# Performance work log

Measured on AMD Instinct MI355X. Metric: run time of the kernel, lower is better.

## Reference

```python
import jax, jax.numpy as jnp
import numpy as np

B, T, D, H, NH = 128, 64, 64, 128, 4


def setup_inputs() -> dict:
    key = jax.random.key(0)
    ks = jax.random.split(key, 32)
    s = 0.05
    inp = {
        "x": jax.random.normal(ks[0], (B, T, D), dtype=jnp.float32),
        "mask": jnp.ones((B, T), dtype=jnp.int32),
        # per-feature GRU params (input size 1, PyTorch gate order r,z,n)
        "Wih": jax.random.normal(ks[1], (D, 3 * H), dtype=jnp.float32) * s,
        "Whh": jax.random.normal(ks[2], (D, 3 * H, H), dtype=jnp.float32) * s,
        "bih": jax.random.normal(ks[3], (D, 3 * H), dtype=jnp.float32) * s,
        "bhh": jax.random.normal(ks[4], (D, 3 * H), dtype=jnp.float32) * s,
        # MHA projections (stored [in,out]; y = x @ W + b)
        "Wq": jax.random.normal(ks[5], (H, H), dtype=jnp.float32) * s,
        "bq": jnp.zeros((H,), dtype=jnp.float32),
        "Wk": jax.random.normal(ks[6], (H, H), dtype=jnp.float32) * s,
        "bk": jnp.zeros((H,), dtype=jnp.float32),
        "Wv": jax.random.normal(ks[7], (H, H), dtype=jnp.float32) * s,
        "bv": jnp.zeros((H,), dtype=jnp.float32),
        "Wo": jax.random.normal(ks[8], (H, H), dtype=jnp.float32) * s,
        "bo": jnp.zeros((H,), dtype=jnp.float32),
        # FFN
        "W1": jax.random.normal(ks[9], (H, 2 * H), dtype=jnp.float32) * s,
        "b1": jnp.zeros((2 * H,), dtype=jnp.float32),
        "W2": jax.random.normal(ks[10], (2 * H, H), dtype=jnp.float32) * s,
        "b2": jnp.zeros((H,), dtype=jnp.float32),
        # LayerNorms
        "g1": jnp.ones((H,), dtype=jnp.float32),
        "be1": jnp.zeros((H,), dtype=jnp.float32),
        "g2": jnp.ones((H,), dtype=jnp.float32),
        "be2": jnp.zeros((H,), dtype=jnp.float32),
        # FinalAttentionQKV
        "Fq": jax.random.normal(ks[11], (H, H), dtype=jnp.float32) * s,
        "fbq": jnp.zeros((H,), dtype=jnp.float32),
        "Fk": jax.random.normal(ks[12], (H, H), dtype=jnp.float32) * s,
        "fbk": jnp.zeros((H,), dtype=jnp.float32),
        "Fv": jax.random.normal(ks[13], (H, H), dtype=jnp.float32) * s,
        "fbv": jnp.zeros((H,), dtype=jnp.float32),
        "Fout": jax.random.normal(ks[14], (H,), dtype=jnp.float32) * s,
        "fbout": jnp.zeros((), dtype=jnp.float32),
    }
    return inp


def _layernorm(x, g, b, eps=1e-5):
    m = jnp.mean(x, axis=-1, keepdims=True)
    v = jnp.mean((x - m) ** 2, axis=-1, keepdims=True)
    return (x - m) * jax.lax.rsqrt(v + eps) * g + b


def _forward(x, mask, Wih, Whh, bih, bhh, Wq, bq, Wk, bk, Wv, bv, Wo, bo,
             W1, b1, W2, b2, g1, be1, g2, be2,
             Fq, fbq, Fk, fbk, Fv, fbv, Fout, fbout):
    Bc, Tc, Dc = x.shape
    Hc = Whh.shape[-1]

    # --- D independent GRUs, fused: batch axes (B, D), scalar input per step ---
    def step(h, xt):  # h: [B,D,H], xt: [B,D]
        gx = xt[..., None] * Wih + bih                     # [B,D,3H]
        gh = jnp.einsum('bdh,dkh->bdk', h, Whh) + bhh      # [B,D,3H]
        r = jax.nn.sigmoid(gx[..., :Hc] + gh[..., :Hc])
        z = jax.nn.sigmoid(gx[..., Hc:2 * Hc] + gh[..., Hc:2 * Hc])
        n = jnp.tanh(gx[..., 2 * Hc:] + r * gh[..., 2 * Hc:])
        hn = (1.0 - z) * n + z * h
        return hn, hn

    xs = jnp.transpose(x, (1, 0, 2))                        # [T,B,D]
    h0 = jnp.zeros((Bc, Dc, Hc), dtype=x.dtype)
    _, ys = jax.lax.scan(step, h0, xs)                      # [T,B,D,H]

    # last_by_lengths: gather hidden state at index lengths-1 per batch element
    lengths = jnp.sum(mask, axis=1)                         # [B]
    idx = jnp.clip(lengths - 1, 0, Tc - 1)
    emb = ys[idx, jnp.arange(Bc)]                           # [B,D,H] (D tokens)

    # --- MHA (self-attention over D feature tokens); dropout = identity (eval) ---
    dk = Hc // NH
    def split_heads(t):
        return jnp.transpose(t.reshape(Bc, Dc, NH, dk), (0, 2, 1, 3))  # [B,NH,D,dk]
    q = split_heads(emb @ Wq + bq)
    k = split_heads(emb @ Wk + bk)
    v = split_heads(emb @ Wv + bv)
    scores = jnp.einsum('bhnd,bhmd->bhnm', q, k) / jnp.sqrt(jnp.float32(dk))
    attn = jax.nn.softmax(scores, axis=-1)
    o = jnp.einsum('bhnm,bhmd->bhnd', attn, v)
    o = jnp.transpose(o, (0, 2, 1, 3)).reshape(Bc, Dc, Hc)
    mha_out = o @ Wo + bo

    h1 = _layernorm(emb + mha_out, g1, be1)
    ffn = jax.nn.relu(h1 @ W1 + b1) @ W2 + b2
    h2 = _layernorm(h1 + ffn, g2, be2)

    # --- FinalAttentionQKV ---
    fq = (h2[:, -1, :] @ Fq + fbq)[:, None, :]              # [B,1,H]
    fk = h2 @ Fk + fbk                                      # [B,D,H]
    fv = h2 @ Fv + fbv                                      # [B,D,H]
    e = jnp.tanh(fq + fk) @ Fout + fbout                    # [B,D]
    a = jax.nn.softmax(e, axis=-1)
    return jnp.einsum('bn,bnh->bh', a, fv)                  # [B,H]


def reference(x, mask, Wih, Whh, bih, bhh, Wq, bq, Wk, bk, Wv, bv, Wo, bo,
              W1, b1, W2, b2, g1, be1, g2, be2,
              Fq, fbq, Fk, fbk, Fv, fbv, Fout, fbout):
    return _forward(x, mask, Wih, Whh, bih, bhh, Wq, bq, Wk, bk, Wv, bv, Wo, bo,
                    W1, b1, W2, b2, g1, be1, g2, be2,
                    Fq, fbq, Fk, fbk, Fv, fbv, Fout, fbout)
```

## Files before the change

### kernel.cpp

```cpp
#include <hip/hip_runtime.h>
#include <hip/hip_bf16.h>
#include <math.h>

#define BB 128
#define TT 64
#define DD 64
#define HH 128
#define NHH 4
#define K3H 384

typedef __attribute__((ext_vector_type(8))) short short8_t;
typedef __attribute__((ext_vector_type(4))) float float4_t;

#define LOG2E 1.4426950408889634f

__device__ __forceinline__ unsigned short f2bf(float f) {
    unsigned int u = __float_as_uint(f);
    u += 0x7fffu + ((u >> 16) & 1u);
    return (unsigned short)(u >> 16);
}

__device__ __forceinline__ unsigned pack_bf2(float lo, float hi) {
    return (unsigned)f2bf(lo) | ((unsigned)f2bf(hi) << 16);
}

__device__ __forceinline__ unsigned pack_bf2_hw(float lo, float hi) {
    __hip_bfloat162 p = __float22bfloat162_rn(make_float2(lo, hi));
    unsigned u;
    __builtin_memcpy(&u, &p, 4);
    return u;
}

__device__ __forceinline__ float bf2f(unsigned short s) {
    return __uint_as_float((unsigned)s << 16);
}

__device__ __forceinline__ float2 pk_fma(float2 a, float2 b, float2 c) {
    return make_float2(fmaf(a.x, b.x, c.x), fmaf(a.y, b.y, c.y));
}
__device__ __forceinline__ float2 pk_sub(float2 a, float2 b) {
    return make_float2(a.x - b.x, a.y - b.y);
}

__global__ __launch_bounds__(512, 4) void gru_mfma_kernel(
    const float* __restrict__ x, const int* __restrict__ mask,
    const float* __restrict__ Wih, const float* __restrict__ Whh,
    const float* __restrict__ bih, const float* __restrict__ bhh,
    float* __restrict__ emb)
{
    const int d  = blockIdx.x;
    const int b0 = blockIdx.y * 16;
    const int tid = threadIdx.x;
    const int w = tid >> 6;
    const int l = tid & 63;
    const int m = l & 15;
    const int q = l >> 4;

    __shared__ __align__(16) unsigned short hbuf[2][16][136];
    __shared__ float xs_t[TT][16];
    __shared__ int tstar_s[16];

    for (int idx = tid; idx < 16 * TT; idx += 512) {
        int t = idx >> 4, row = idx & 15;
        xs_t[t][row] = x[((size_t)(b0 + row) * TT + t) * DD + d];
    }
    if (tid < 16) {
        int b = b0 + tid, len = 0;
        for (int t = 0; t < TT; ++t) len += mask[b * TT + t];
        int ts = len - 1;
        if (ts < 0) ts = 0;
        if (ts > TT - 1) ts = TT - 1;
        tstar_s[tid] = ts;
    }
    for (int idx = tid; idx < 16 * 136; idx += 512)
        ((unsigned short*)hbuf)[idx] = 0;

    short8_t Wf[3][4];
#pragma unroll
    for (int g = 0; g < 3; ++g) {
        float sc = (g == 2) ? (2.f * LOG2E) : (-LOG2E);
        int kcol = g * HH + 16 * w + m;
        const float* wrow = Whh + ((size_t)d * K3H + kcol) * HH;
#pragma unroll
        for (int kc = 0; kc < 4; ++kc) {
            int j0 = kc * 32 + q * 8;
            float4 w0 = *(const float4*)(wrow + j0);
            float4 w1 = *(const float4*)(wrow + j0 + 4);
            short8_t f;
            f[0] = (short)f2bf(w0.x * sc); f[1] = (short)f2bf(w0.y * sc);
            f[2] = (short)f2bf(w0.z * sc); f[3] = (short)f2bf(w0.w * sc);
            f[4] = (short)f2bf(w1.x * sc); f[5] = (short)f2bf(w1.y * sc);
            f[6] = (short)f2bf(w1.z * sc); f[7] = (short)f2bf(w1.w * sc);
            Wf[g][kc] = f;
        }
    }

    const int hcol0 = 16 * w + q * 4;
    float4 wr4 = *(const float4*)&Wih[d * K3H + hcol0];
    float4 wz4 = *(const float4*)&Wih[d * K3H + HH + hcol0];
    float4 wn4 = *(const float4*)&Wih[d * K3H + 2 * HH + hcol0];
    float4 br4 = *(const float4*)&bih[d * K3H + hcol0];
    float4 bz4 = *(const float4*)&bih[d * K3H + HH + hcol0];
    float4 bni4 = *(const float4*)&bih[d * K3H + 2 * HH + hcol0];
    float4 bhr4 = *(const float4*)&bhh[d * K3H + hcol0];
    float4 bhz4 = *(const float4*)&bhh[d * K3H + HH + hcol0];
    float4 bnh4 = *(const float4*)&bhh[d * K3H + 2 * HH + hcol0];
    float brs[4], bzs[4], bnis[4], bnhs[4], wrs[4], wzs[4], wns[4];
#pragma unroll
    for (int r = 0; r < 4; ++r) {
        wrs[r] = -LOG2E * ((const float*)&wr4)[r];
        wzs[r] = -LOG2E * ((const float*)&wz4)[r];
        wns[r] = 2.f * LOG2E * ((const float*)&wn4)[r];
        brs[r] = -LOG2E * (((const float*)&br4)[r] + ((const float*)&bhr4)[r]);
        bzs[r] = -LOG2E * (((const float*)&bz4)[r] + ((const float*)&bhz4)[r]);
        bnis[r] = 2.f * LOG2E * ((const float*)&bni4)[r];
        bnhs[r] = 2.f * LOG2E * ((const float*)&bnh4)[r];
    }

    float hprev[4];
#pragma unroll
    for (int i = 0; i < 4; ++i) hprev[i] = 0.f;

    __syncthreads();
    const int tstar_m = tstar_s[m];
    float* embp = emb + (((size_t)(b0 + m)) * DD + d) * HH + hcol0;

    for (int t = 0; t < TT; ++t) {
        const unsigned short* hb = &hbuf[t & 1][0][0];
        unsigned short* hbn = &hbuf[(t & 1) ^ 1][0][0];

        short8_t hf[4];
#pragma unroll
        for (int kc = 0; kc < 4; ++kc)
            hf[kc] = *(const short8_t*)(hb + m * 136 + kc * 32 + q * 8);
        float xv = xs_t[t][m];

        float4_t ar = {brs[0], brs[1], brs[2], brs[3]};
        float4_t az = {bzs[0], bzs[1], bzs[2], bzs[3]};
        float4_t an = {bnhs[0], bnhs[1], bnhs[2], bnhs[3]};
#pragma unroll
        for (int kc = 0; kc < 4; ++kc) {
            ar = __builtin_amdgcn_mfma_f32_16x16x32_bf16(Wf[0][kc], hf[kc], ar, 0, 0, 0);
            az = __builtin_amdgcn_mfma_f32_16x16x32_bf16(Wf[1][kc], hf[kc], az, 0, 0, 0);
            an = __builtin_amdgcn_mfma_f32_16x16x32_bf16(Wf[2][kc], hf[kc], an, 0, 0, 0);
        }

        float hn4[4];
        float2 xv2 = make_float2(xv, xv);
#pragma unroll
        for (int pp = 0; pp < 2; ++pp) {
            const int r0 = 2 * pp, r1 = r0 + 1;
            float2 grs = pk_fma(xv2, make_float2(wrs[r0], wrs[r1]),
                                make_float2(ar[r0], ar[r1]));
            float2 gzs = pk_fma(xv2, make_float2(wzs[r0], wzs[r1]),
                                make_float2(az[r0], az[r1]));
            float2 rg = make_float2(
                __builtin_amdgcn_rcpf(1.f + __builtin_amdgcn_exp2f(grs.x)),
                __builtin_amdgcn_rcpf(1.f + __builtin_amdgcn_exp2f(grs.y)));
            float2 zg = make_float2(
                __builtin_amdgcn_rcpf(1.f + __builtin_amdgcn_exp2f(gzs.x)),
                __builtin_amdgcn_rcpf(1.f + __builtin_amdgcn_exp2f(gzs.y)));
            float2 gns = pk_fma(rg, make_float2(an[r0], an[r1]),
                                pk_fma(xv2, make_float2(wns[r0], wns[r1]),
                                       make_float2(bnis[r0], bnis[r1])));
            float2 tn = make_float2(
                fmaf(-2.f, __builtin_amdgcn_rcpf(__builtin_amdgcn_exp2f(gns.x) + 1.f), 1.f),
                fmaf(-2.f, __builtin_amdgcn_rcpf(__builtin_amdgcn_exp2f(gns.y) + 1.f), 1.f));
            float2 hp = make_float2(hprev[r0], hprev[r1]);
            float2 hn = pk_fma(zg, pk_sub(hp, tn), tn);
            hprev[r0] = hn.x; hprev[r1] = hn.y;
            hn4[r0] = hn.x; hn4[r1] = hn.y;
        }
        uint2 uu;
        uu.x = pack_bf2_hw(hn4[0], hn4[1]);
        uu.y = pack_bf2_hw(hn4[2], hn4[3]);
        *(uint2*)(hbn + m * 136 + hcol0) = uu;
        if (t == tstar_m) {
            float4 hv; hv.x = hn4[0]; hv.y = hn4[1]; hv.z = hn4[2]; hv.w = hn4[3];
            *(float4*)embp = hv;
        }
        __syncthreads();
    }
}

__device__ __forceinline__ void load_wfrag(const float* __restrict__ Wp, int N,
                                           int col, float scale, int q,
                                           short8_t fr[4])
{
#pragma unroll
    for (int kc = 0; kc < 4; ++kc) {
        const float* p = Wp + (size_t)(kc * 32 + q * 8) * N + col;
        short8_t f;
#pragma unroll
        for (int j = 0; j < 8; ++j)
            f[j] = (short)f2bf(p[(size_t)j * N] * scale);
        fr[kc] = f;
    }
}

__device__ __forceinline__ void load_afrag(const unsigned short (*S)[136],
                                           short8_t Af[4][4], int m16, int q)
{
#pragma unroll
    for (int mt = 0; mt < 4; ++mt)
#pragma unroll
        for (int kc = 0; kc < 4; ++kc)
            Af[mt][kc] = *(const short8_t*)&S[mt * 16 + m16][kc * 32 + q * 8];
}

__device__ __forceinline__ void mm_regw(short8_t Af[4][4], short8_t Bf[4],
                                        float4_t acc[4])
{
#pragma unroll
    for (int mt = 0; mt < 4; ++mt) {
        float4_t a = acc[mt];
#pragma unroll
        for (int kc = 0; kc < 4; ++kc)
            a = __builtin_amdgcn_mfma_f32_16x16x32_bf16(Af[mt][kc], Bf[kc], a, 0, 0, 0);
        acc[mt] = a;
    }
}

__device__ __forceinline__ void zero4(float4_t acc[4]) {
#pragma unroll
    for (int mt = 0; mt < 4; ++mt) acc[mt] = (float4_t){0.f, 0.f, 0.f, 0.f};
}

__device__ __forceinline__ void store_rows(unsigned short (*Dst)[136], float4_t acc[4],
                                           float bv, int relu, int col, int q)
{
#pragma unroll
    for (int mt = 0; mt < 4; ++mt)
#pragma unroll
        for (int reg = 0; reg < 4; ++reg) {
            float v = acc[mt][reg] + bv;
            if (relu) v = fmaxf(v, 0.f);
            Dst[mt * 16 + q * 4 + reg][col] = f2bf(v);
        }
}

__global__ __launch_bounds__(512) void tail_kernel(
    const float* __restrict__ emb,
    const float* __restrict__ Wq, const float* __restrict__ bq,
    const float* __restrict__ Wk, const float* __restrict__ bk,
    const float* __restrict__ Wv, const float* __restrict__ bv,
    const float* __restrict__ Wo, const float* __restrict__ bo,
    const float* __restrict__ W1, const float* __restrict__ b1,
    const float* __restrict__ W2, const float* __restrict__ b2,
    const float* __restrict__ g1, const float* __restrict__ be1,
    const float* __restrict__ g2, const float* __restrict__ be2,
    const float* __restrict__ Fq, const float* __restrict__ fbq,
    const float* __restrict__ Fk, const float* __restrict__ fbk,
    const float* __restrict__ Fv, const float* __restrict__ fbv,
    const float* __restrict__ Fout, const float* __restrict__ fbout,
    float* __restrict__ out)
{
    const int b = blockIdx.x;
    const int tid = threadIdx.x;
    const int w = tid >> 6, l = tid & 63, m16 = l & 15, q = l >> 4;
    const int col = w * 16 + m16;

    __shared__ __align__(16) unsigned short E[64][136];
    __shared__ __align__(16) unsigned short Qs[64][136];
    __shared__ __align__(16) unsigned short Ks[64][136];
    __shared__ __align__(16) unsigned short Vt[128][72];
    __shared__ float sc4[4][64][66];
    __shared__ float lnp[64][8], lnp2[64][8];
    __shared__ float mean_s[64], rs_s[64];
    __shared__ float fq_s[128], fo_s[128], e_s[64], red_s[256];

    const float* embB = emb + (size_t)b * 64 * 128;
    const float SS = 0.17677669529663687f;

    short8_t WqF[4], WkF[4], WvF[4];
    load_wfrag(Wq, 128, col, SS, q, WqF);
    load_wfrag(Wk, 128, col, 1.f, q, WkF);
    load_wfrag(Wv, 128, col, 1.f, q, WvF);
    float bqv = bq[col] * SS, bkv = bk[col], bvv = bv[col];

    for (int it = tid; it < 2048; it += 512) {
        int r = it >> 5, c4 = (it & 31) << 2;
        float4 a = *(const float4*)&embB[r * 128 + c4];
        uint2 p; p.x = pack_bf2(a.x, a.y); p.y = pack_bf2(a.z, a.w);
        *(uint2*)&E[r][c4] = p;
    }
    __syncthreads();

    short8_t Af[4][4];
    float4_t acc[4];
    load_afrag(E, Af, m16, q);

    zero4(acc); mm_regw(Af, WqF, acc); store_rows(Qs, acc, bqv, 0, col, q);
    zero4(acc); mm_regw(Af, WkF, acc); store_rows(Ks, acc, bkv, 0, col, q);
    zero4(acc); mm_regw(Af, WvF, acc);
#pragma unroll
    for (int mt = 0; mt < 4; ++mt) {
        uint2 pk;
        pk.x = pack_bf2(acc[mt][0] + bvv, acc[mt][1] + bvv);
        pk.y = pack_bf2(acc[mt][2] + bvv, acc[mt][3] + bvv);
        *(uint2*)&Vt[col][mt * 16 + q * 4] = pk;
    }
    __syncthreads();

    short8_t WoF[4], W1aF[4], W1bF[4];
    load_wfrag(Wo, 128, col, 1.f, q, WoF);
    load_wfrag(W1, 256, col, 1.f, q, W1aF);
    load_wfrag(W1, 256, 128 + col, 1.f, q, W1bF);
    float bov = bo[col], b1a = b1[col], b1b = b1[128 + col];
    float g1v = g1[col], be1v = be1[col];

    {
        int hd = w >> 1, ntb = (w & 1) * 2;
#pragma unroll
        for (int mt = 0; mt < 4; ++mt) {
            short8_t Aq = *(const short8_t*)&Qs[mt * 16 + m16][hd * 32 + q * 8];
#pragma unroll
            for (int nn = 0; nn < 2; ++nn) {
                int nt = ntb + nn;
                short8_t Bk = *(const short8_t*)&Ks[nt * 16 + m16][hd * 32 + q * 8];
                float4_t a = {0.f, 0.f, 0.f, 0.f};
                a = __builtin_amdgcn_mfma_f32_16x16x32_bf16(Aq, Bk, a, 0, 0, 0);
#pragma unroll
                for (int reg = 0; reg < 4; ++reg)
                    sc4[hd][mt * 16 + q * 4 + reg][nt * 16 + m16] = a[reg];
            }
        }
    }
    __syncthreads();

    {
        int pr = tid >> 1, hd2 = pr >> 6, row = pr & 63, half = (tid & 1) * 32;
        float v[32]; float mx = -1e30f;
#pragma unroll
        for (int c = 0; c < 32; ++c) { v[c] = sc4[hd2][row][half + c]; mx = fmaxf(mx, v[c]); }
        mx = fmaxf(mx, __shfl_xor(mx, 1));
        float sum = 0.f;
#pragma unroll
        for (int c = 0; c < 32; ++c) { v[c] = __expf(v[c] - mx); sum += v[c]; }
        sum += __shfl_xor(sum, 1);
        float inv = __builtin_amdgcn_rcpf(sum);
        unsigned short (*Pd)[136] = (hd2 < 2) ? Qs : Ks;
        int cb = (hd2 & 1) * 64 + half;
#pragma unroll
        for (int c = 0; c < 16; ++c)
            *(unsigned*)&Pd[row][cb + 2 * c] = pack_bf2(v[2 * c] * inv, v[2 * c + 1] * inv);
    }
    __syncthreads();

    {
        int hd = w >> 1, nt = w & 1;
        const unsigned short (*P)[136] = (hd < 2) ? (const unsigned short (*)[136])Qs
                                                  : (const unsigned short (*)[136])Ks;
        int pb = (hd & 1) * 64;
        int vrow = hd * 32 + nt * 16 + m16;
        short8_t B0f = *(const short8_t*)&Vt[vrow][q * 8];
        short8_t B1f = *(const short8_t*)&Vt[vrow][32 + q * 8];
#pragma unroll
        for (int mt = 0; mt < 4; ++mt) {
            short8_t A0 = *(const short8_t*)&P[mt * 16 + m16][pb + q * 8];
            short8_t A1 = *(const short8_t*)&P[mt * 16 + m16][pb + 32 + q * 8];
            float4_t a = {0.f, 0.f, 0.f, 0.f};
            a = __builtin_amdgcn_mfma_f32_16x16x32_bf16(A0, B0f, a, 0, 0, 0);
            a = __builtin_amdgcn_mfma_f32_16x16x32_bf16(A1, B1f, a, 0, 0, 0);
#pragma unroll
            for (int reg = 0; reg < 4; ++reg)
                E[mt * 16 + q * 4 + reg][vrow] = f2bf(a[reg]);
        }
    }
    __syncthreads();

    short8_t W2aF[4], W2bF[4], FkF[4], FvF[4];
    load_wfrag(W2, 128, col, 1.f, q, W2aF);
    load_wfrag(W2 + (size_t)128 * 128, 128, col, 1.f, q, W2bF);
    load_wfrag(Fk, 128, col, 1.f, q, FkF);
    load_wfrag(Fv, 128, col, 1.f, q, FvF);
    float b2v = b2[col], fbkv = fbk[col], fbvv = fbv[col];
    float g2v = g2[col], be2v = be2[col];

    load_afrag(E, Af, m16, q);
    zero4(acc); mm_regw(Af, WoF, acc);
    float h1v[4][4];
#pragma unroll
    for (int mt = 0; mt < 4; ++mt)
#pragma unroll
        for (int reg = 0; reg < 4; ++reg) {
            int row = mt * 16 + q * 4 + reg;
            h1v[mt][reg] = acc[mt][reg] + bov + embB[(size_t)row * 128 + col];
        }
#pragma unroll
    for (int mt = 0; mt < 4; ++mt)
#pragma unroll
        for (int reg = 0; reg < 4; ++reg) {
            float s = h1v[mt][reg], s2 = s * s;
            s += __shfl_xor(s, 1); s += __shfl_xor(s, 2); s += __shfl_xor(s, 4); s += __shfl_xor(s, 8);
            s2 += __shfl_xor(s2, 1); s2 += __shfl_xor(s2, 2); s2 += __shfl_xor(s2, 4); s2 += __shfl_xor(s2, 8);
            if (m16 == 0) { int row = mt * 16 + q * 4 + reg; lnp[row][w] = s; lnp2[row][w] = s2; }
        }
    __syncthreads();
    if (tid < 64) {
        float s = 0.f, s2 = 0.f;
#pragma unroll
        for (int k = 0; k < 8; ++k) { s += lnp[tid][k]; s2 += lnp2[tid][k]; }
        float mn = s * (1.f / 128.f);
        mean_s[tid] = mn;
        rs_s[tid] = rsqrtf(s2 * (1.f / 128.f) - mn * mn + 1e-5f);
    }
    __syncthreads();
#pragma unroll
    for (int mt = 0; mt < 4; ++mt)
#pragma unroll
        for (int reg = 0; reg < 4; ++reg) {
            int row = mt * 16 + q * 4 + reg;
            float hv = (h1v[mt][reg] - mean_s[row]) * rs_s[row] * g1v + be1v;
            h1v[mt][reg] = hv;
            E[row][col] = f2bf(hv);
        }
    __syncthreads();

    load_afrag(E, Af, m16, q);
    zero4(acc); mm_regw(Af, W1aF, acc); store_rows(Qs, acc, b1a, 1, col, q);
    zero4(acc); mm_regw(Af, W1bF, acc); store_rows(Ks, acc, b1b, 1, col, q);
    __syncthreads();

    {
        short8_t AfQ[4][4], AfK[4][4];
        load_afrag(Qs, AfQ, m16, q);
        load_afrag(Ks, AfK, m16, q);
        zero4(acc); mm_regw(AfQ, W2aF, acc); mm_regw(AfK, W2bF, acc);
    }
#pragma unroll
    for (int mt = 0; mt < 4; ++mt)
#pragma unroll
        for (int reg = 0; reg < 4; ++reg)
            h1v[mt][reg] = acc[mt][reg] + b2v + h1v[mt][reg];
#pragma unroll
    for (int mt = 0; mt < 4; ++mt)
#pragma unroll
        for (int reg = 0; reg < 4; ++reg) {
            float s = h1v[mt][reg], s2 = s * s;
            s += __shfl_xor(s, 1); s += __shfl_xor(s, 2); s += __shfl_xor(s, 4); s += __shfl_xor(s, 8);
            s2 += __shfl_xor(s2, 1); s2 += __shfl_xor(s2, 2); s2 += __shfl_xor(s2, 4); s2 += __shfl_xor(s2, 8);
            if (m16 == 0) { int row = mt * 16 + q * 4 + reg; lnp[row][w] = s; lnp2[row][w] = s2; }
        }
    __syncthreads();
    if (tid < 64) {
        float s = 0.f, s2 = 0.f;
#pragma unroll
        for (int k = 0; k < 8; ++k) { s += lnp[tid][k]; s2 += lnp2[tid][k]; }
        float mn = s * (1.f / 128.f);
        mean_s[tid] = mn;
        rs_s[tid] = rsqrtf(s2 * (1.f / 128.f) - mn * mn + 1e-5f);
    }
    __syncthreads();
#pragma unroll
    for (int mt = 0; mt < 4; ++mt)
#pragma unroll
        for (int reg = 0; reg < 4; ++reg) {
            int row = mt * 16 + q * 4 + reg;
            float hv = (h1v[mt][reg] - mean_s[row]) * rs_s[row] * g2v + be2v;
            E[row][col] = f2bf(hv);
        }
    __syncthreads();

    load_afrag(E, Af, m16, q);
    zero4(acc); mm_regw(Af, FkF, acc); store_rows(Qs, acc, fbkv, 0, col, q);
    zero4(acc); mm_regw(Af, FvF, acc); store_rows(Ks, acc, fbvv, 0, col, q);
    {
        int co = tid >> 2, sub = tid & 3;
        float a2 = 0.f;
#pragma unroll 8
        for (int mm2 = sub * 32; mm2 < sub * 32 + 32; ++mm2)
            a2 = fmaf(bf2f(E[63][mm2]), Fq[(size_t)mm2 * 128 + co], a2);
        a2 += __shfl_xor(a2, 1);
        a2 += __shfl_xor(a2, 2);
        if (sub == 0) fq_s[co] = a2 + fbq[co];
    }
    if (tid < 128) fo_s[tid] = Fout[tid];
    __syncthreads();

    {
        int dd = tid >> 3, c8 = tid & 7;
        float p = 0.f;
#pragma unroll
        for (int c = 0; c < 16; ++c) {
            int cc = c8 * 16 + c;
            float t = fq_s[cc] + bf2f(Qs[dd][cc]);
            float tn = 1.f - 2.f * __builtin_amdgcn_rcpf(
                __builtin_amdgcn_exp2f(2.f * LOG2E * t) + 1.f);
            p = fmaf(tn, fo_s[cc], p);
        }
        p += __shfl_xor(p, 1); p += __shfl_xor(p, 2); p += __shfl_xor(p, 4);
        if (c8 == 0) e_s[dd] = p + fbout[0];
    }
    __syncthreads();
    if (tid < 64) {
        float e = e_s[tid], mx = e;
        for (int o = 32; o; o >>= 1) mx = fmaxf(mx, __shfl_xor(mx, o));
        float pe = __expf(e - mx);
        float s = pe;
        for (int o = 32; o; o >>= 1) s += __shfl_xor(s, o);
        e_s[tid] = pe / s;
    }
    __syncthreads();
    if (tid < 256) {
        int c2 = tid & 127, rg2 = tid >> 7;
        float a = 0.f;
        for (int d2 = rg2 * 32; d2 < rg2 * 32 + 32; ++d2)
            a = fmaf(e_s[d2], bf2f(Ks[d2][c2]), a);
        red_s[tid] = a;
    }
    __syncthreads();
    if (tid < 128)
        out[(size_t)b * 128 + tid] = red_s[tid] + red_s[tid + 128];
}

extern "C" void kernel_launch(void* const* d_in, const int* in_sizes, int n_in,
                              void* d_out, int out_size, void* d_ws, size_t ws_size,
                              hipStream_t stream)
{
    const float* x    = (const float*)d_in[0];
    const int*   mask = (const int*)d_in[1];
    const float* Wih  = (const float*)d_in[2];
    const float* Whh  = (const float*)d_in[3];
    const float* bih  = (const float*)d_in[4];
    const float* bhh  = (const float*)d_in[5];
    const float* Wq = (const float*)d_in[6];   const float* bq = (const float*)d_in[7];
    const float* Wk = (const float*)d_in[8];   const float* bk = (const float*)d_in[9];
    const float* Wv = (const float*)d_in[10];  const float* bv = (const float*)d_in[11];
    const float* Wo = (const float*)d_in[12];  const float* bo = (const float*)d_in[13];
    const float* W1 = (const float*)d_in[14];  const float* b1 = (const float*)d_in[15];
    const float* W2 = (const float*)d_in[16];  const float* b2 = (const float*)d_in[17];
    const float* g1 = (const float*)d_in[18];  const float* be1 = (const float*)d_in[19];
    const float* g2 = (const float*)d_in[20];  const float* be2 = (const float*)d_in[21];
    const float* Fq = (const float*)d_in[22];  const float* fbq = (const float*)d_in[23];
    const float* Fk = (const float*)d_in[24];  const float* fbk = (const float*)d_in[25];
    const float* Fv = (const float*)d_in[26];  const float* fbv = (const float*)d_in[27];
    const float* Fout = (const float*)d_in[28]; const float* fbout = (const float*)d_in[29];
    float* out = (float*)d_out;
    float* ws  = (float*)d_ws;

    float* emb = ws;

    gru_mfma_kernel<<<dim3(DD, BB / 16), 512, 0, stream>>>(x, mask, Wih, Whh, bih, bhh, emb);
    tail_kernel<<<BB, 512, 0, stream>>>(
        emb, Wq, bq, Wk, bk, Wv, bv, Wo, bo, W1, b1, W2, b2,
        g1, be1, g2, be2, Fq, fbq, Fk, fbk, Fv, fbv, Fout, fbout, out);
}
```

Before: 243.7 us.

## Halve GRU block to 4 waves each computing two 16-column tiles

```diff
diff --git a/kernel.cpp b/kernel.cpp
--- a/kernel.cpp
+++ b/kernel.cpp
@@ -42,7 +42,7 @@
     return make_float2(a.x - b.x, a.y - b.y);
 }
 
-__global__ __launch_bounds__(512, 4) void gru_mfma_kernel(
+__global__ __launch_bounds__(256, 2) void gru_mfma_kernel(
     const float* __restrict__ x, const int* __restrict__ mask,
     const float* __restrict__ Wih, const float* __restrict__ Whh,
     const float* __restrict__ bih, const float* __restrict__ bhh,
@@ -59,8 +59,10 @@
     __shared__ __align__(16) unsigned short hbuf[2][16][136];
     __shared__ float xs_t[TT][16];
     __shared__ int tstar_s[16];
-
-    for (int idx = tid; idx < 16 * TT; idx += 512) {
+    __shared__ char lds_pad_[41 * 1024];
+    if (mask[0] == 0x7abcdef) ((volatile char*)lds_pad_)[0] = 1;
+
+    for (int idx = tid; idx < 16 * TT; idx += 256) {
         int t = idx >> 4, row = idx & 15;
         xs_t[t][row] = x[((size_t)(b0 + row) * TT + t) * DD + d];
     }
@@ -72,58 +74,68 @@
         if (ts > TT - 1) ts = TT - 1;
         tstar_s[tid] = ts;
     }
-    for (int idx = tid; idx < 16 * 136; idx += 512)
+    for (int idx = tid; idx < 16 * 136; idx += 256)
         ((unsigned short*)hbuf)[idx] = 0;
 
-    short8_t Wf[3][4];
+    short8_t Wf[3][2][4];
 #pragma unroll
     for (int g = 0; g < 3; ++g) {
         float sc = (g == 2) ? (2.f * LOG2E) : (-LOG2E);
-        int kcol = g * HH + 16 * w + m;
-        const float* wrow = Whh + ((size_t)d * K3H + kcol) * HH;
-#pragma unroll
-        for (int kc = 0; kc < 4; ++kc) {
-            int j0 = kc * 32 + q * 8;
-            float4 w0 = *(const float4*)(wrow + j0);
-            float4 w1 = *(const float4*)(wrow + j0 + 4);
-            short8_t f;
-            f[0] = (short)f2bf(w0.x * sc); f[1] = (short)f2bf(w0.y * sc);
-            f[2] = (short)f2bf(w0.z * sc); f[3] = (short)f2bf(w0.w * sc);
-            f[4] = (short)f2bf(w1.x * sc); f[5] = (short)f2bf(w1.y * sc);
-            f[6] = (short)f2bf(w1.z * sc); f[7] = (short)f2bf(w1.w * sc);
-            Wf[g][kc] = f;
-        }
-    }
-
-    const int hcol0 = 16 * w + q * 4;
-    float4 wr4 = *(const float4*)&Wih[d * K3H + hcol0];
-    float4 wz4 = *(const float4*)&Wih[d * K3H + HH + hcol0];
-    float4 wn4 = *(const float4*)&Wih[d * K3H + 2 * HH + hcol0];
-    float4 br4 = *(const float4*)&bih[d * K3H + hcol0];
-    float4 bz4 = *(const float4*)&bih[d * K3H + HH + hcol0];
-    float4 bni4 = *(const float4*)&bih[d * K3H + 2 * HH + hcol0];
-    float4 bhr4 = *(const float4*)&bhh[d * K3H + hcol0];
-    float4 bhz4 = *(const float4*)&bhh[d * K3H + HH + hcol0];
-    float4 bnh4 = *(const float4*)&bhh[d * K3H + 2 * HH + hcol0];
-    float brs[4], bzs[4], bnis[4], bnhs[4], wrs[4], wzs[4], wns[4];
-#pragma unroll
-    for (int r = 0; r < 4; ++r) {
-        wrs[r] = -LOG2E * ((const float*)&wr4)[r];
-        wzs[r] = -LOG2E * ((const float*)&wz4)[r];
-        wns[r] = 2.f * LOG2E * ((const float*)&wn4)[r];
-        brs[r] = -LOG2E * (((const float*)&br4)[r] + ((const float*)&bhr4)[r]);
-        bzs[r] = -LOG2E * (((const float*)&bz4)[r] + ((const float*)&bhz4)[r]);
-        bnis[r] = 2.f * LOG2E * ((const float*)&bni4)[r];
-        bnhs[r] = 2.f * LOG2E * ((const float*)&bnh4)[r];
-    }
-
-    float hprev[4];
-#pragma unroll
-    for (int i = 0; i < 4; ++i) hprev[i] = 0.f;
+#pragma unroll
+        for (int i = 0; i < 2; ++i) {
+            int kcol = g * HH + 32 * w + 16 * i + m;
+            const float* wrow = Whh + ((size_t)d * K3H + kcol) * HH;
+#pragma unroll
+            for (int kc = 0; kc < 4; ++kc) {
+                int j0 = kc * 32 + q * 8;
+                float4 w0 = *(const float4*)(wrow + j0);
+                float4 w1 = *(const float4*)(wrow + j0 + 4);
+                short8_t f;
+                f[0] = (short)f2bf(w0.x * sc); f[1] = (short)f2bf(w0.y * sc);
+                f[2] = (short)f2bf(w0.z * sc); f[3] = (short)f2bf(w0.w * sc);
+                f[4] = (short)f2bf(w1.x * sc); f[5] = (short)f2bf(w1.y * sc);
+                f[6] = (short)f2bf(w1.z * sc); f[7] = (short)f2bf(w1.w * sc);
+                Wf[g][i][kc] = f;
+            }
+        }
+    }
+
+    float brs[2][4], bzs[2][4], bnis[2][4], bnhs[2][4];
+    float wrs[2][4], wzs[2][4], wns[2][4];
+#pragma unroll
+    for (int i = 0; i < 2; ++i) {
+        const int hc = 32 * w + 16 * i + 4 * q;
+        float4 wr4  = *(const float4*)&Wih[d * K3H + hc];
+        float4 wz4  = *(const float4*)&Wih[d * K3H + HH + hc];
+        float4 wn4  = *(const float4*)&Wih[d * K3H + 2 * HH + hc];
+        float4 br4  = *(const float4*)&bih[d * K3H + hc];
+        float4 bz4  = *(const float4*)&bih[d * K3H + HH + hc];
+        float4 bni4 = *(const float4*)&bih[d * K3H + 2 * HH + hc];
+        float4 bhr4 = *(const float4*)&bhh[d * K3H + hc];
+        float4 bhz4 = *(const float4*)&bhh[d * K3H + HH + hc];
+        float4 bnh4 = *(const float4*)&bhh[d * K3H + 2 * HH + hc];
+#pragma unroll
+        for (int r = 0; r < 4; ++r) {
+            wrs[i][r]  = -LOG2E * ((const float*)&wr4)[r];
+            wzs[i][r]  = -LOG2E * ((const float*)&wz4)[r];
+            wns[i][r]  = 2.f * LOG2E * ((const float*)&wn4)[r];
+            brs[i][r]  = -LOG2E * (((const float*)&br4)[r] + ((const float*)&bhr4)[r]);
+            bzs[i][r]  = -LOG2E * (((const float*)&bz4)[r] + ((const float*)&bhz4)[r]);
+            bnis[i][r] = 2.f * LOG2E * ((const float*)&bni4)[r];
+            bnhs[i][r] = 2.f * LOG2E * ((const float*)&bnh4)[r];
+        }
+    }
+
+    float hprev[2][4];
+#pragma unroll
+    for (int i = 0; i < 2; ++i)
+#pragma unroll
+        for (int r = 0; r < 4; ++r) hprev[i][r] = 0.f;
 
     __syncthreads();
     const int tstar_m = tstar_s[m];
-    float* embp = emb + (((size_t)(b0 + m)) * DD + d) * HH + hcol0;
+    float* embp0 = emb + (((size_t)(b0 + m)) * DD + d) * HH + 32 * w + 4 * q;
+    float* embp1 = embp0 + 16;
 
     for (int t = 0; t < TT; ++t) {
         const unsigned short* hb = &hbuf[t & 1][0][0];
@@ -135,49 +147,58 @@
             hf[kc] = *(const short8_t*)(hb + m * 136 + kc * 32 + q * 8);
         float xv = xs_t[t][m];
 
-        float4_t ar = {brs[0], brs[1], brs[2], brs[3]};
-        float4_t az = {bzs[0], bzs[1], bzs[2], bzs[3]};
-        float4_t an = {bnhs[0], bnhs[1], bnhs[2], bnhs[3]};
-#pragma unroll
-        for (int kc = 0; kc < 4; ++kc) {
-            ar = __builtin_amdgcn_mfma_f32_16x16x32_bf16(Wf[0][kc], hf[kc], ar, 0, 0, 0);
-            az = __builtin_amdgcn_mfma_f32_16x16x32_bf16(Wf[1][kc], hf[kc], az, 0, 0, 0);
-            an = __builtin_amdgcn_mfma_f32_16x16x32_bf16(Wf[2][kc], hf[kc], an, 0, 0, 0);
-        }
-
-        float hn4[4];
+        float4_t ar[2], az[2], an[2];
+#pragma unroll
+        for (int i = 0; i < 2; ++i) {
+            ar[i] = (float4_t){brs[i][0], brs[i][1], brs[i][2], brs[i][3]};
+            az[i] = (float4_t){bzs[i][0], bzs[i][1], bzs[i][2], bzs[i][3]};
+            an[i] = (float4_t){bnhs[i][0], bnhs[i][1], bnhs[i][2], bnhs[i][3]};
+        }
+#pragma unroll
+        for (int kc = 0; kc < 4; ++kc)
+#pragma unroll
+            for (int i = 0; i < 2; ++i) {
+                ar[i] = __builtin_amdgcn_mfma_f32_16x16x32_bf16(Wf[0][i][kc], hf[kc], ar[i], 0, 0, 0);
+                az[i] = __builtin_amdgcn_mfma_f32_16x16x32_bf16(Wf[1][i][kc], hf[kc], az[i], 0, 0, 0);
+                an[i] = __builtin_amdgcn_mfma_f32_16x16x32_bf16(Wf[2][i][kc], hf[kc], an[i], 0, 0, 0);
+            }
+
         float2 xv2 = make_float2(xv, xv);
 #pragma unroll
-        for (int pp = 0; pp < 2; ++pp) {
-            const int r0 = 2 * pp, r1 = r0 + 1;
-            float2 grs = pk_fma(xv2, make_float2(wrs[r0], wrs[r1]),
-                                make_float2(ar[r0], ar[r1]));
-            float2 gzs = pk_fma(xv2, make_float2(wzs[r0], wzs[r1]),
-                                make_float2(az[r0], az[r1]));
-            float2 rg = make_float2(
-                __builtin_amdgcn_rcpf(1.f + __builtin_amdgcn_exp2f(grs.x)),
-                __builtin_amdgcn_rcpf(1.f + __builtin_amdgcn_exp2f(grs.y)));
-            float2 zg = make_float2(
-                __builtin_amdgcn_rcpf(1.f + __builtin_amdgcn_exp2f(gzs.x)),
-                __builtin_amdgcn_rcpf(1.f + __builtin_amdgcn_exp2f(gzs.y)));
-            float2 gns = pk_fma(rg, make_float2(an[r0], an[r1]),
-                                pk_fma(xv2, make_float2(wns[r0], wns[r1]),
-                                       make_float2(bnis[r0], bnis[r1])));
-            float2 tn = make_float2(
-                fmaf(-2.f, __builtin_amdgcn_rcpf(__builtin_amdgcn_exp2f(gns.x) + 1.f), 1.f),
-                fmaf(-2.f, __builtin_amdgcn_rcpf(__builtin_amdgcn_exp2f(gns.y) + 1.f), 1.f));
-            float2 hp = make_float2(hprev[r0], hprev[r1]);
-            float2 hn = pk_fma(zg, pk_sub(hp, tn), tn);
-            hprev[r0] = hn.x; hprev[r1] = hn.y;
-            hn4[r0] = hn.x; hn4[r1] = hn.y;
-        }
-        uint2 uu;
-        uu.x = pack_bf2_hw(hn4[0], hn4[1]);
-        uu.y = pack_bf2_hw(hn4[2], hn4[3]);
-        *(uint2*)(hbn + m * 136 + hcol0) = uu;
-        if (t == tstar_m) {
-            float4 hv; hv.x = hn4[0]; hv.y = hn4[1]; hv.z = hn4[2]; hv.w = hn4[3];
-            *(float4*)embp = hv;
+        for (int i = 0; i < 2; ++i) {
+            float hn4[4];
+#pragma unroll
+            for (int pp = 0; pp < 2; ++pp) {
+                const int r0 = 2 * pp, r1 = r0 + 1;
+                float2 grs = pk_fma(xv2, make_float2(wrs[i][r0], wrs[i][r1]),
+                                    make_float2(ar[i][r0], ar[i][r1]));
+                float2 gzs = pk_fma(xv2, make_float2(wzs[i][r0], wzs[i][r1]),
+                                    make_float2(az[i][r0], az[i][r1]));
+                float2 rg = make_float2(
+                    __builtin_amdgcn_rcpf(1.f + __builtin_amdgcn_exp2f(grs.x)),
+                    __builtin_amdgcn_rcpf(1.f + __builtin_amdgcn_exp2f(grs.y)));
+                float2 zg = make_float2(
+                    __builtin_amdgcn_rcpf(1.f + __builtin_amdgcn_exp2f(gzs.x)),
+                    __builtin_amdgcn_rcpf(1.f + __builtin_amdgcn_exp2f(gzs.y)));
+                float2 gns = pk_fma(rg, make_float2(an[i][r0], an[i][r1]),
+                                    pk_fma(xv2, make_float2(wns[i][r0], wns[i][r1]),
+                                           make_float2(bnis[i][r0], bnis[i][r1])));
+                float2 tn = make_float2(
+                    fmaf(-2.f, __builtin_amdgcn_rcpf(__builtin_amdgcn_exp2f(gns.x) + 1.f), 1.f),
+                    fmaf(-2.f, __builtin_amdgcn_rcpf(__builtin_amdgcn_exp2f(gns.y) + 1.f), 1.f));
+                float2 hp = make_float2(hprev[i][r0], hprev[i][r1]);
+                float2 hn = pk_fma(zg, pk_sub(hp, tn), tn);
+                hprev[i][r0] = hn.x; hprev[i][r1] = hn.y;
+                hn4[r0] = hn.x; hn4[r1] = hn.y;
+            }
+            uint2 uu;
+            uu.x = pack_bf2_hw(hn4[0], hn4[1]);
+            uu.y = pack_bf2_hw(hn4[2], hn4[3]);
+            *(uint2*)(hbn + m * 136 + 32 * w + 16 * i + 4 * q) = uu;
+            if (t == tstar_m) {
+                float4 hv; hv.x = hn4[0]; hv.y = hn4[1]; hv.z = hn4[2]; hv.w = hn4[3];
+                *(float4*)(i ? embp1 : embp0) = hv;
+            }
         }
         __syncthreads();
     }
@@ -541,7 +562,7 @@
 
     float* emb = ws;
 
-    gru_mfma_kernel<<<dim3(DD, BB / 16), 512, 0, stream>>>(x, mask, Wih, Whh, bih, bhh, emb);
+    gru_mfma_kernel<<<dim3(DD, BB / 16), 256, 0, stream>>>(x, mask, Wih, Whh, bih, bhh, emb);
     tail_kernel<<<BB, 512, 0, stream>>>(
         emb, Wq, bq, Wk, bk, Wv, bv, Wo, bo, W1, b1, W2, b2,
         g1, be1, g2, be2, Fq, fbq, Fk, fbk, Fv, fbv, Fout, fbout, out);
```

After: 253.2 us. 3.9% more time.

## Process two 16-row batch groups per GRU block to reuse weight fragments

Applied to the files above, without the earlier changes.

```diff
diff --git a/kernel.cpp b/kernel.cpp
--- a/kernel.cpp
+++ b/kernel.cpp
@@ -42,29 +42,63 @@
     return make_float2(a.x - b.x, a.y - b.y);
 }
 
-__global__ __launch_bounds__(512, 4) void gru_mfma_kernel(
+__device__ __forceinline__ void gru_epilogue(
+    const float4_t& ar, const float4_t& az, const float4_t& an, float xv,
+    const float wrs[4], const float wzs[4], const float wns[4],
+    const float bnis[4], float hprev[4], float hn4[4])
+{
+    float2 xv2 = make_float2(xv, xv);
+#pragma unroll
+    for (int pp = 0; pp < 2; ++pp) {
+        const int r0 = 2 * pp, r1 = r0 + 1;
+        float2 grs = pk_fma(xv2, make_float2(wrs[r0], wrs[r1]),
+                            make_float2(ar[r0], ar[r1]));
+        float2 gzs = pk_fma(xv2, make_float2(wzs[r0], wzs[r1]),
+                            make_float2(az[r0], az[r1]));
+        float2 rg = make_float2(
+            __builtin_amdgcn_rcpf(1.f + __builtin_amdgcn_exp2f(grs.x)),
+            __builtin_amdgcn_rcpf(1.f + __builtin_amdgcn_exp2f(grs.y)));
+        float2 zg = make_float2(
+            __builtin_amdgcn_rcpf(1.f + __builtin_amdgcn_exp2f(gzs.x)),
+            __builtin_amdgcn_rcpf(1.f + __builtin_amdgcn_exp2f(gzs.y)));
+        float2 gns = pk_fma(rg, make_float2(an[r0], an[r1]),
+                            pk_fma(xv2, make_float2(wns[r0], wns[r1]),
+                                   make_float2(bnis[r0], bnis[r1])));
+        float2 tn = make_float2(
+            fmaf(-2.f, __builtin_amdgcn_rcpf(__builtin_amdgcn_exp2f(gns.x) + 1.f), 1.f),
+            fmaf(-2.f, __builtin_amdgcn_rcpf(__builtin_amdgcn_exp2f(gns.y) + 1.f), 1.f));
+        float2 hp = make_float2(hprev[r0], hprev[r1]);
+        float2 hn = pk_fma(zg, pk_sub(hp, tn), tn);
+        hprev[r0] = hn.x; hprev[r1] = hn.y;
+        hn4[r0] = hn.x; hn4[r1] = hn.y;
+    }
+}
+
+__global__ __launch_bounds__(512, 2) void gru_mfma_kernel(
     const float* __restrict__ x, const int* __restrict__ mask,
     const float* __restrict__ Wih, const float* __restrict__ Whh,
     const float* __restrict__ bih, const float* __restrict__ bhh,
     float* __restrict__ emb)
 {
     const int d  = blockIdx.x;
-    const int b0 = blockIdx.y * 16;
+    const int b0 = blockIdx.y * 32;
     const int tid = threadIdx.x;
     const int w = tid >> 6;
     const int l = tid & 63;
     const int m = l & 15;
     const int q = l >> 4;
 
-    __shared__ __align__(16) unsigned short hbuf[2][16][136];
-    __shared__ float xs_t[TT][16];
-    __shared__ int tstar_s[16];
-
-    for (int idx = tid; idx < 16 * TT; idx += 512) {
-        int t = idx >> 4, row = idx & 15;
+    __shared__ __align__(16) unsigned short hbuf[2][2][16][136];
+    __shared__ float xs_t[TT][32];
+    __shared__ int tstar_s[32];
+    __shared__ char lds_pad_[30 * 1024];
+    if (mask[0] == 0x7abcdef) ((volatile char*)lds_pad_)[0] = 1;
+
+    for (int idx = tid; idx < 32 * TT; idx += 512) {
+        int t = idx >> 5, row = idx & 31;
         xs_t[t][row] = x[((size_t)(b0 + row) * TT + t) * DD + d];
     }
-    if (tid < 16) {
+    if (tid < 32) {
         int b = b0 + tid, len = 0;
         for (int t = 0; t < TT; ++t) len += mask[b * TT + t];
         int ts = len - 1;
@@ -72,7 +106,7 @@
         if (ts > TT - 1) ts = TT - 1;
         tstar_s[tid] = ts;
     }
-    for (int idx = tid; idx < 16 * 136; idx += 512)
+    for (int idx = tid; idx < 2 * 2 * 16 * 136; idx += 512)
         ((unsigned short*)hbuf)[idx] = 0;
 
     short8_t Wf[3][4];
@@ -117,67 +151,67 @@
         bnhs[r] = 2.f * LOG2E * ((const float*)&bnh4)[r];
     }
 
-    float hprev[4];
-#pragma unroll
-    for (int i = 0; i < 4; ++i) hprev[i] = 0.f;
-
-    __syncthreads();
-    const int tstar_m = tstar_s[m];
-    float* embp = emb + (((size_t)(b0 + m)) * DD + d) * HH + hcol0;
+    float hprevA[4], hprevB[4];
+#pragma unroll
+    for (int i = 0; i < 4; ++i) { hprevA[i] = 0.f; hprevB[i] = 0.f; }
+
+    __syncthreads();
+    const int tstarA = tstar_s[m];
+    const int tstarB = tstar_s[16 + m];
+    float* embpA = emb + (((size_t)(b0 + m)) * DD + d) * HH + hcol0;
+    float* embpB = emb + (((size_t)(b0 + 16 + m)) * DD + d) * HH + hcol0;
 
     for (int t = 0; t < TT; ++t) {
-        const unsigned short* hb = &hbuf[t & 1][0][0];
-        unsigned short* hbn = &hbuf[(t & 1) ^ 1][0][0];
-
-        short8_t hf[4];
-#pragma unroll
-        for (int kc = 0; kc < 4; ++kc)
-            hf[kc] = *(const short8_t*)(hb + m * 136 + kc * 32 + q * 8);
-        float xv = xs_t[t][m];
-
-        float4_t ar = {brs[0], brs[1], brs[2], brs[3]};
-        float4_t az = {bzs[0], bzs[1], bzs[2], bzs[3]};
-        float4_t an = {bnhs[0], bnhs[1], bnhs[2], bnhs[3]};
+        const int par = t & 1;
+
+        short8_t hfA[4], hfB[4];
 #pragma unroll
         for (int kc = 0; kc < 4; ++kc) {
-            ar = __builtin_amdgcn_mfma_f32_16x16x32_bf16(Wf[0][kc], hf[kc], ar, 0, 0, 0);
-            az = __builtin_amdgcn_mfma_f32_16x16x32_bf16(Wf[1][kc], hf[kc], az, 0, 0, 0);
-            an = __builtin_amdgcn_mfma_f32_16x16x32_bf16(Wf[2][kc], hf[kc], an, 0, 0, 0);
+            hfA[kc] = *(const short8_t*)&hbuf[0][par][m][kc * 32 + q * 8];
+            hfB[kc] = *(const short8_t*)&hbuf[1][par][m][kc * 32 + q * 8];
+        }
+        float xvA = xs_t[t][m];
+        float xvB = xs_t[t][16 + m];
+
+        float4_t arA = {brs[0], brs[1], brs[2], brs[3]};
+        float4_t azA = {bzs[0], bzs[1], bzs[2], bzs[3]};
+        float4_t anA = {bnhs[0], bnhs[1], bnhs[2], bnhs[3]};
+        float4_t arB = arA, azB = azA, anB = anA;
+#pragma unroll
+        for (int kc = 0; kc < 4; ++kc) {
+            arA = __builtin_amdgcn_mfma_f32_16x16x32_bf16(Wf[0][kc], hfA[kc], arA, 0, 0, 0);
+            azA = __builtin_amdgcn_mfma_f32_16x16x32_bf16(Wf[1][kc], hfA[kc], azA, 0, 0, 0);
+            anA = __builtin_amdgcn_mfma_f32_16x16x32_bf16(Wf[2][kc], hfA[kc], anA, 0, 0, 0);
+        }
+#pragma unroll
+        for (int kc = 0; kc < 4; ++kc) {
+            arB = __builtin_amdgcn_mfma_f32_16x16x32_bf16(Wf[0][kc], hfB[kc], arB, 0, 0, 0);
+            azB = __builtin_amdgcn_mfma_f32_16x16x32_bf16(Wf[1][kc], hfB[kc], azB, 0, 0, 0);
+            anB = __builtin_amdgcn_mfma_f32_16x16x32_bf16(Wf[2][kc], hfB[kc], anB, 0, 0, 0);
         }
 
         float hn4[4];
-        float2 xv2 = make_float2(xv, xv);
-#pragma unroll
-        for (int pp = 0; pp < 2; ++pp) {
-            const int r0 = 2 * pp, r1 = r0 + 1;
-            float2 grs = pk_fma(xv2, make_float2(wrs[r0], wrs[r1]),
-                                make_float2(ar[r0], ar[r1]));
-            float2 gzs = pk_fma(xv2, make_float2(wzs[r0], wzs[r1]),
-                                make_float2(az[r0], az[r1]));
-            float2 rg = make_float2(
-                __builtin_amdgcn_rcpf(1.f + __builtin_amdgcn_exp2f(grs.x)),
-                __builtin_amdgcn_rcpf(1.f + __builtin_amdgcn_exp2f(grs.y)));
-            float2 zg = make_float2(
-                __builtin_amdgcn_rcpf(1.f + __builtin_amdgcn_exp2f(gzs.x)),
-                __builtin_amdgcn_rcpf(1.f + __builtin_amdgcn_exp2f(gzs.y)));
-            float2 gns = pk_fma(rg, make_float2(an[r0], an[r1]),
-                                pk_fma(xv2, make_float2(wns[r0], wns[r1]),
-                                       make_float2(bnis[r0], bnis[r1])));
-            float2 tn = make_float2(
-                fmaf(-2.f, __builtin_amdgcn_rcpf(__builtin_amdgcn_exp2f(gns.x) + 1.f), 1.f),
-                fmaf(-2.f, __builtin_amdgcn_rcpf(__builtin_amdgcn_exp2f(gns.y) + 1.f), 1.f));
-            float2 hp = make_float2(hprev[r0], hprev[r1]);
-            float2 hn = pk_fma(zg, pk_sub(hp, tn), tn);
-            hprev[r0] = hn.x; hprev[r1] = hn.y;
-            hn4[r0] = hn.x; hn4[r1] = hn.y;
-        }
-        uint2 uu;
-        uu.x = pack_bf2_hw(hn4[0], hn4[1]);
-        uu.y = pack_bf2_hw(hn4[2], hn4[3]);
-        *(uint2*)(hbn + m * 136 + hcol0) = uu;
-        if (t == tstar_m) {
-            float4 hv; hv.x = hn4[0]; hv.y = hn4[1]; hv.z = hn4[2]; hv.w = hn4[3];
-            *(float4*)embp = hv;
+        gru_epilogue(arA, azA, anA, xvA, wrs, wzs, wns, bnis, hprevA, hn4);
+        {
+            uint2 uu;
+            uu.x = pack_bf2_hw(hn4[0], hn4[1]);
+            uu.y = pack_bf2_hw(hn4[2], hn4[3]);
+            *(uint2*)&hbuf[0][par ^ 1][m][hcol0] = uu;
+            if (t == tstarA) {
+                float4 hv; hv.x = hn4[0]; hv.y = hn4[1]; hv.z = hn4[2]; hv.w = hn4[3];
+                *(float4*)embpA = hv;
+            }
+        }
+        gru_epilogue(arB, azB, anB, xvB, wrs, wzs, wns, bnis, hprevB, hn4);
+        {
+            uint2 uu;
+            uu.x = pack_bf2_hw(hn4[0], hn4[1]);
+            uu.y = pack_bf2_hw(hn4[2], hn4[3]);
+            *(uint2*)&hbuf[1][par ^ 1][m][hcol0] = uu;
+            if (t == tstarB) {
+                float4 hv; hv.x = hn4[0]; hv.y = hn4[1]; hv.z = hn4[2]; hv.w = hn4[3];
+                *(float4*)embpB = hv;
+            }
         }
         __syncthreads();
     }
@@ -541,7 +575,7 @@
 
     float* emb = ws;
 
-    gru_mfma_kernel<<<dim3(DD, BB / 16), 512, 0, stream>>>(x, mask, Wih, Whh, bih, bhh, emb);
+    gru_mfma_kernel<<<dim3(DD, BB / 32), 512, 0, stream>>>(x, mask, Wih, Whh, bih, bhh, emb);
     tail_kernel<<<BB, 512, 0, stream>>>(
         emb, Wq, bq, Wk, bk, Wv, bv, Wo, bo, W1, b1, W2, b2,
         g1, be1, g2, be2, Fq, fbq, Fk, fbk, Fv, fbv, Fout, fbout, out);
```

New measurement: 241.2 us. About the same (-1.0%).
